# Optimization experiments

Measured on AMD Instinct MI355X. Metric: run time of the kernel, lower is better.

## Reference

```python
import jax, jax.numpy as jnp
import numpy as np

N = 100000      # nodes
E = 1600000     # edges (avg degree 16)
D = 128         # input feature dim
UNITS = 64      # ChebyNet units
K = 3           # Chebyshev order
C = 40          # num_classes
LMAX = 2.0      # lambda_max for rw-normalized Laplacian


def setup_inputs() -> dict:
    key = jax.random.key(0)
    ks = jax.random.split(key, 6)
    x = jax.random.normal(ks[0], (N, D), dtype=jnp.float32)
    edge_index = jax.random.randint(ks[1], (2, E), 0, N, dtype=jnp.int32)
    edge_weight = jax.random.uniform(ks[2], (E,), dtype=jnp.float32)
    W = jax.random.normal(ks[3], (K, D, UNITS), dtype=jnp.float32) * 0.05   # per-order Cheb kernels
    b = jnp.zeros((UNITS,), dtype=jnp.float32)
    Wd = jax.random.normal(ks[4], (UNITS, C), dtype=jnp.float32) * 0.05     # final Dense
    bd = jnp.zeros((C,), dtype=jnp.float32)
    return {"x": x, "edge_index": edge_index, "edge_weight": edge_weight,
            "W": W, "b": b, "Wd": Wd, "bd": bd}


def reference(x, edge_index, edge_weight, W, b, Wd, bd):
    src, dst = edge_index[0], edge_index[1]
    # rw normalization: A_hat = D^{-1} A, deg computed at dst
    deg = jax.ops.segment_sum(edge_weight, dst, num_segments=N)
    w_norm = edge_weight / jnp.maximum(deg[dst], 1e-12)  # [E]

    def lhat(h):
        # L h = h - D^{-1} A h ; L_hat = (2/lmax) L - I
        ah = jax.ops.segment_sum(h[src] * w_norm[:, None], dst, num_segments=N)  # [N, D]
        return (2.0 / LMAX) * (h - ah) - h

    # Chebyshev recursion T_0 = x, T_1 = L_hat x, T_2 = 2 L_hat T_1 - T_0
    T0 = x
    T1 = lhat(T0)
    T2 = 2.0 * lhat(T1) - T0
    h = T0 @ W[0] + T1 @ W[1] + T2 @ W[2] + b  # [N, UNITS]
    return h @ Wd + bd                          # [N, C]
```

## Files before the change

### kernel.cpp

```cpp
#include <hip/hip_runtime.h>

namespace {
constexpr int N = 100000;
constexpr int E = 1600000;
constexpr int D = 128;
constexpr int U = 64;
constexpr int C = 40;
constexpr int C2 = C / 2;
constexpr int RP = 32;
constexpr int SLOTS = 64;
constexpr int NB = (N + 255) / 256;
constexpr int CAP = 4608;
constexpr int EPB = 16;
constexpr int TPB = 256;
constexpr int GK = 136;
constexpr int PROJ_BLOCKS = (N + 63) / 64;

constexpr size_t OFF_BCUR = 0;
constexpr size_t OFF_META = OFF_BCUR + 512;
constexpr size_t OFF_CSR = OFF_META + (size_t)2 * N;
constexpr size_t OFF_BBUF = OFF_CSR + (size_t)2 * N * SLOTS;
constexpr size_t BBUF_INTS = (size_t)NB * CAP * 2;
constexpr size_t OFF_P1 = OFF_BBUF + BBUF_INTS;
constexpr size_t OFF_P2B = OFF_P1 + (size_t)N * C + 32;
constexpr size_t OFF_RBF = OFF_P2B + (size_t)N * RP;
constexpr size_t OFF_GBF = OFF_RBF + (size_t)N * RP;
constexpr size_t OFF_BC = OFF_GBF + 128 * GK / 2;

constexpr int SMEM_FUSED = 64 * GK * 2 + 256;
}

__device__ inline unsigned f2bf(float x) {
    unsigned u = __float_as_uint(x);
    return (u + 0x7fffu + ((u >> 16) & 1u)) >> 16;
}
__device__ inline unsigned pack_bf2(float a, float b) { return f2bf(a) | (f2bf(b) << 16); }
__device__ inline float2 unpack_bf2(unsigned v) {
    return make_float2(__uint_as_float(v << 16), __uint_as_float(v & 0xffff0000u));
}

typedef __attribute__((ext_vector_type(8))) short bf16x8;
typedef __attribute__((ext_vector_type(4))) float f32x4;

__global__ void prep_weights(const float* __restrict__ W, const float* __restrict__ b,
                             const float* __restrict__ Wd, const float* __restrict__ bd,
                             unsigned short* __restrict__ Gbf, float* __restrict__ bc,
                             int* __restrict__ bcur) {
    if (blockIdx.x == 0) {
        for (int i = threadIdx.x; i < 512; i += 256) bcur[i] = 0;
    }
    int t = blockIdx.x * blockDim.x + threadIdx.x;
    if (t < 128 * 128) {
        int n = t >> 7, k = t & 127;
        float s = 0.f;
        if (n < 40) {
            const float* W0 = W + (size_t)k * U;
            const float* W2 = W + (size_t)2 * D * U + (size_t)k * U;
            for (int u = 0; u < U; ++u) s += (W0[u] - W2[u]) * Wd[u * C + n];
        } else if (n < 80) {
            const float* W1 = W + (size_t)D * U + (size_t)k * U;
            for (int u = 0; u < U; ++u) s -= W1[u] * Wd[u * C + (n - 40)];
        } else if (n < 120) {
            const float* W2 = W + (size_t)2 * D * U + (size_t)k * U;
            for (int u = 0; u < U; ++u) s += 2.f * W2[u] * Wd[u * C + (n - 80)];
        }
        Gbf[n * GK + k] = (unsigned short)f2bf(s);
    } else if (t < 128 * 128 + C) {
        int c = t - 128 * 128;
        float s = bd[c];
        for (int u = 0; u < U; ++u) s += b[u] * Wd[u * C + c];
        bc[c] = s;
    }
}

__global__ __launch_bounds__(TPB) void bucket_scatter(const int* __restrict__ src,
                                                      const int* __restrict__ dst,
                                                      const float* __restrict__ ew,
                                                      int* __restrict__ bcur,
                                                      int2* __restrict__ bbuf2) {
    __shared__ int hist[NB];
    __shared__ int base[NB];
    int t = threadIdx.x;
    for (int i = t; i < NB; i += TPB) hist[i] = 0;
    __syncthreads();

    size_t e0 = (size_t)blockIdx.x * (TPB * EPB);
    int ms[EPB], md[EPB], mw[EPB], mr[EPB];
#pragma unroll
    for (int k = 0; k < EPB; ++k) {
        size_t e = e0 + (size_t)k * TPB + t;
        if (e < E) {
            ms[k] = src[e];
            md[k] = dst[e];
            mw[k] = __float_as_int(ew[e]);
            mr[k] = atomicAdd(&hist[md[k] >> 8], 1);
        } else {
            md[k] = -1;
        }
    }
    __syncthreads();
    for (int i = t; i < NB; i += TPB) {
        int c = hist[i];
        base[i] = c ? atomicAdd(&bcur[i], c) : 0;
    }
    __syncthreads();
#pragma unroll
    for (int k = 0; k < EPB; ++k) {
        if (md[k] >= 0) {
            int bkt = md[k] >> 8;
            int slot = base[bkt] + mr[k];
            if (slot < CAP)
                bbuf2[(size_t)bkt * CAP + slot] =
                    make_int2(ms[k] | ((md[k] & 255) << 24), mw[k]);
        }
    }
}

__global__ __launch_bounds__(256) void csr_and_proj(
    const int* __restrict__ bcur, const int2* __restrict__ bbuf2,
    int2* __restrict__ meta, int2* __restrict__ csr,
    const float* __restrict__ X, const unsigned short* __restrict__ Gbf,
    const float* __restrict__ bc, float* __restrict__ out,
    float* __restrict__ P1, unsigned short* __restrict__ P2B16) {
    __shared__ __align__(16) unsigned char smem[SMEM_FUSED];
    int t = threadIdx.x;

    if (blockIdx.x < NB) {
        int* lcur = (int*)smem;
        float* lw = (float*)(smem + 1024);
        int b = blockIdx.x;
        lcur[t] = 0;
        lw[t] = 0.f;
        __syncthreads();
        int cnt = min(bcur[b], CAP);
        const int2* bb = bbuf2 + (size_t)b * CAP;
        for (int i = t; i < cnt; i += 256) {
            int2 r = bb[i];
            int idx = ((unsigned)r.x) >> 24;
            int slot = atomicAdd(&lcur[idx], 1);
            atomicAdd(&lw[idx], __int_as_float(r.y));
            if (slot < SLOTS)
                csr[(((size_t)(b << 8) + idx) << 6) + slot] =
                    make_int2(r.x & 0x00FFFFFF, r.y);
        }
        __syncthreads();
        int node = (b << 8) + t;
        if (node < N) {
            int c = min(lcur[t], SLOTS);
            float rdeg = 1.f / fmaxf(lw[t], 1e-12f);
            meta[node] = make_int2(c, __float_as_int(rdeg));
            int padded = min((c + 15) & ~15, SLOTS);
            for (int s = c; s < padded; ++s)
                csr[((size_t)node << 6) + s] = make_int2(0, 0);
        }
        return;
    }

    int rb = blockIdx.x - NB;
    unsigned short* a_s = (unsigned short*)smem;
    float* bc_s = (float*)(smem + 64 * GK * 2);
    if (t < C) bc_s[t] = bc[t];

#pragma unroll
    for (int i = 0; i < 8; ++i) {
        int idx = i * 256 + t;
        int row = idx >> 5, kq = idx & 31;
        size_t grow = (size_t)rb * 64 + row;
        float4 v = (grow < N) ? ((const float4*)X)[grow * 32 + kq]
                              : make_float4(0.f, 0.f, 0.f, 0.f);
        unsigned* dstp = (unsigned*)(a_s + row * GK + kq * 4);
        dstp[0] = pack_bf2(v.x, v.y);
        dstp[1] = pack_bf2(v.z, v.w);
    }
    __syncthreads();

    int w = t >> 6, l = t & 63;
    int lr = l & 15, lh = l >> 4;

    bf16x8 afr[4];
#pragma unroll
    for (int ks = 0; ks < 4; ++ks)
        afr[ks] = *(const bf16x8*)(a_s + (w * 16 + lr) * GK + ks * 32 + lh * 8);

    f32x4 acc[8];
#pragma unroll
    for (int tt = 0; tt < 8; ++tt) {
        acc[tt] = (f32x4){0.f, 0.f, 0.f, 0.f};
#pragma unroll
        for (int ks = 0; ks < 4; ++ks) {
            bf16x8 bfr = *(const bf16x8*)(Gbf + (tt * 16 + lr) * GK + ks * 32 + lh * 8);
            acc[tt] = __builtin_amdgcn_mfma_f32_16x16x32_bf16(afr[ks], bfr, acc[tt], 0, 0, 0);
        }
    }

#pragma unroll
    for (int tt = 0; tt < 8; ++tt) {
        int gcol = tt * 16 + lr;
#pragma unroll
        for (int r = 0; r < 4; ++r) {
            size_t grow = (size_t)rb * 64 + w * 16 + lh * 4 + r;
            if (grow >= N) continue;
            float v = acc[tt][r];
            if (gcol < 40) {
                out[grow * C + gcol] = v + bc_s[gcol];
            } else if (gcol < 80) {
                P1[grow * C + (gcol - 40)] = v;
            } else if (gcol < 120) {
                P2B16[grow * 64 + (gcol - 80)] = (unsigned short)f2bf(v);
            }
        }
    }
}

template <bool OUT_BF>
__global__ __launch_bounds__(256) void spmm40v4(const int2* __restrict__ meta,
                                                const int2* __restrict__ csr,
                                                const unsigned* __restrict__ Xg,
                                                const float* __restrict__ Add,
                                                void* __restrict__ Yv) {
    int wid = (blockIdx.x * blockDim.x + threadIdx.x) >> 6;
    if (wid >= N) return;
    int uw = __builtin_amdgcn_readfirstlane(wid);
    int2 m = meta[uw];
    int c = m.x;
    float rdeg = __int_as_float(m.y);
    const int2* __restrict__ row = csr + ((size_t)uw << 6);
    int lane = threadIdx.x & 63;
    bool hi = lane >= 32;
    unsigned voff = (unsigned)(lane & 31);

    float2 ad = make_float2(0.f, 0.f);
    if (lane < C2) ad = ((const float2*)Add)[(size_t)wid * C2 + lane];

    float2 acc = make_float2(0.f, 0.f);
    for (int j0 = 0; j0 < c; j0 += 16) {
        unsigned va[8];
        float wa[8];
#pragma unroll
        for (int k = 0; k < 8; ++k) {
            int2 a = row[j0 + k];
            int2 b = row[j0 + 8 + k];
            int col = hi ? b.x : a.x;
            wa[k] = __int_as_float(hi ? b.y : a.y);
            va[k] = Xg[((unsigned)col << 5) + voff];
        }
#pragma unroll
        for (int k = 0; k < 8; ++k) {
            float2 v = unpack_bf2(va[k]);
            acc.x = fmaf(wa[k], v.x, acc.x);
            acc.y = fmaf(wa[k], v.y, acc.y);
        }
    }
    acc.x += __shfl_xor(acc.x, 32);
    acc.y += __shfl_xor(acc.y, 32);

    if (OUT_BF) {
        if (lane < 32) {
            unsigned o = 0u;
            if (lane < C2)
                o = pack_bf2(fmaf(acc.x, rdeg, ad.x), fmaf(acc.y, rdeg, ad.y));
            ((unsigned*)Yv)[((size_t)wid << 5) + lane] = o;
        }
    } else {
        if (lane < C2) {
            ((float2*)Yv)[(size_t)wid * C2 + lane] =
                make_float2(fmaf(acc.x, rdeg, ad.x), fmaf(acc.y, rdeg, ad.y));
        }
    }
}

extern "C" void kernel_launch(void* const* d_in, const int* in_sizes, int n_in,
                              void* d_out, int out_size, void* d_ws, size_t ws_size,
                              hipStream_t stream) {
    const float* x = (const float*)d_in[0];
    const int* ei = (const int*)d_in[1];
    const float* ew = (const float*)d_in[2];
    const float* W = (const float*)d_in[3];
    const float* b = (const float*)d_in[4];
    const float* Wd = (const float*)d_in[5];
    const float* bd = (const float*)d_in[6];
    float* out = (float*)d_out;

    const int* src = ei;
    const int* dst = ei + E;

    float* ws = (float*)d_ws;
    int* bcur = (int*)(ws + OFF_BCUR);
    int2* meta = (int2*)(ws + OFF_META);
    int2* csr = (int2*)(ws + OFF_CSR);
    int2* bbuf2 = (int2*)(ws + OFF_BBUF);
    float* P1 = ws + OFF_P1;
    unsigned* P2B = (unsigned*)(ws + OFF_P2B);
    unsigned* Rbf = (unsigned*)(ws + OFF_RBF);
    unsigned short* Gbf = (unsigned short*)(ws + OFF_GBF);
    float* bc = ws + OFF_BC;

    prep_weights<<<(128 * 128 + C + 255) / 256, 256, 0, stream>>>(W, b, Wd, bd, Gbf, bc, bcur);

    bucket_scatter<<<(E + TPB * EPB - 1) / (TPB * EPB), TPB, 0, stream>>>(src, dst, ew, bcur, bbuf2);

    csr_and_proj<<<NB + PROJ_BLOCKS, 256, 0, stream>>>(bcur, bbuf2, meta, csr, x, Gbf, bc,
                                                       out, P1, (unsigned short*)P2B);

    spmm40v4<true><<<((size_t)N * 64 + 255) / 256, 256, 0, stream>>>(meta, csr, P2B, P1, Rbf);
    spmm40v4<false><<<((size_t)N * 64 + 255) / 256, 256, 0, stream>>>(meta, csr, Rbf, out, out);
}
```

Baseline: 135.0 us.

## Process two destination nodes per wavefront in SpMM, one per half-wave

The SpMM kernels now assign a pair of nodes to each 64-lane wavefront, with each 32-lane half handling its own node's full neighbour list. This replaces the old scheme, where the two halves split one node's edges and then combined them with a cross-lane shuffle. CSR padding is extended to the larger degree of each node pair so both halves can loop to a shared bound, and the grid is halved. This removes the shuffle reduction and halves the number of waves. The cost is wasted gathers on zero-padded slots whenever the two paired nodes have different degrees.

Result: no change. 135.6 us (+0.5%).

```diff
diff --git a/kernel.cpp b/kernel.cpp
--- a/kernel.cpp
+++ b/kernel.cpp
@@ -147,9 +147,10 @@
         int node = (b << 8) + t;
         if (node < N) {
             int c = min(lcur[t], SLOTS);
+            int cp = min(lcur[t ^ 1], SLOTS);
             float rdeg = 1.f / fmaxf(lw[t], 1e-12f);
             meta[node] = make_int2(c, __float_as_int(rdeg));
-            int padded = min((c + 15) & ~15, SLOTS);
+            int padded = min((max(c, cp) + 15) & ~15, SLOTS);
             for (int s = c; s < padded; ++s)
                 csr[((size_t)node << 6) + s] = make_int2(0, 0);
         }
@@ -213,57 +214,56 @@
 }
 
 template <bool OUT_BF>
-__global__ __launch_bounds__(256) void spmm40v4(const int2* __restrict__ meta,
+__global__ __launch_bounds__(256) void spmm40v6(const int2* __restrict__ meta,
                                                 const int2* __restrict__ csr,
                                                 const unsigned* __restrict__ Xg,
                                                 const float* __restrict__ Add,
                                                 void* __restrict__ Yv) {
-    int wid = (blockIdx.x * blockDim.x + threadIdx.x) >> 6;
-    if (wid >= N) return;
-    int uw = __builtin_amdgcn_readfirstlane(wid);
-    int2 m = meta[uw];
-    int c = m.x;
-    float rdeg = __int_as_float(m.y);
-    const int2* __restrict__ row = csr + ((size_t)uw << 6);
+    int wpair = (blockIdx.x * blockDim.x + threadIdx.x) >> 6;
+    if (wpair * 2 >= N) return;
+    int uw = __builtin_amdgcn_readfirstlane(wpair);
+    int4 mm = ((const int4*)meta)[uw];
+    int cA = mm.x, cB = mm.z;
     int lane = threadIdx.x & 63;
     bool hi = lane >= 32;
+    int myn = 2 * uw + (hi ? 1 : 0);
+    float rdeg = __int_as_float(hi ? mm.w : mm.y);
+    const int2* __restrict__ rowA = csr + ((size_t)(2 * uw) << 6);
+    const int2* __restrict__ rowB = rowA + SLOTS;
     unsigned voff = (unsigned)(lane & 31);
+    int bound = min((max(cA, cB) + 15) & ~15, SLOTS);
 
     float2 ad = make_float2(0.f, 0.f);
-    if (lane < C2) ad = ((const float2*)Add)[(size_t)wid * C2 + lane];
+    if (voff < C2) ad = ((const float2*)Add)[(size_t)myn * C2 + voff];
 
     float2 acc = make_float2(0.f, 0.f);
-    for (int j0 = 0; j0 < c; j0 += 16) {
-        unsigned va[8];
-        float wa[8];
-#pragma unroll
-        for (int k = 0; k < 8; ++k) {
-            int2 a = row[j0 + k];
-            int2 b = row[j0 + 8 + k];
+    for (int j0 = 0; j0 < bound; j0 += 16) {
+        unsigned va[16];
+        float wa[16];
+#pragma unroll
+        for (int k = 0; k < 16; ++k) {
+            int2 a = rowA[j0 + k];
+            int2 b = rowB[j0 + k];
             int col = hi ? b.x : a.x;
             wa[k] = __int_as_float(hi ? b.y : a.y);
             va[k] = Xg[((unsigned)col << 5) + voff];
         }
 #pragma unroll
-        for (int k = 0; k < 8; ++k) {
+        for (int k = 0; k < 16; ++k) {
             float2 v = unpack_bf2(va[k]);
             acc.x = fmaf(wa[k], v.x, acc.x);
             acc.y = fmaf(wa[k], v.y, acc.y);
         }
     }
-    acc.x += __shfl_xor(acc.x, 32);
-    acc.y += __shfl_xor(acc.y, 32);
 
     if (OUT_BF) {
-        if (lane < 32) {
-            unsigned o = 0u;
-            if (lane < C2)
-                o = pack_bf2(fmaf(acc.x, rdeg, ad.x), fmaf(acc.y, rdeg, ad.y));
-            ((unsigned*)Yv)[((size_t)wid << 5) + lane] = o;
-        }
+        unsigned o = 0u;
+        if (voff < C2)
+            o = pack_bf2(fmaf(acc.x, rdeg, ad.x), fmaf(acc.y, rdeg, ad.y));
+        ((unsigned*)Yv)[((size_t)myn << 5) + voff] = o;
     } else {
-        if (lane < C2) {
-            ((float2*)Yv)[(size_t)wid * C2 + lane] =
+        if (voff < C2) {
+            ((float2*)Yv)[(size_t)myn * C2 + voff] =
                 make_float2(fmaf(acc.x, rdeg, ad.x), fmaf(acc.y, rdeg, ad.y));
         }
     }
@@ -302,6 +302,7 @@
     csr_and_proj<<<NB + PROJ_BLOCKS, 256, 0, stream>>>(bcur, bbuf2, meta, csr, x, Gbf, bc,
                                                        out, P1, (unsigned short*)P2B);
 
-    spmm40v4<true><<<((size_t)N * 64 + 255) / 256, 256, 0, stream>>>(meta, csr, P2B, P1, Rbf);
-    spmm40v4<false><<<((size_t)N * 64 + 255) / 256, 256, 0, stream>>>(meta, csr, Rbf, out, out);
-}
+    int spmm_blocks = (N / 2 * 64 + 255) / 256;
+    spmm40v6<true><<<spmm_blocks, 256, 0, stream>>>(meta, csr, P2B, P1, Rbf);
+    spmm40v6<false><<<spmm_blocks, 256, 0, stream>>>(meta, csr, Rbf, out, out);
+}
```
